# Kernel tuning notes

Measured on AMD Instinct MI355X. Metric: run time of the kernel, lower is better.

## Reference

```python
import jax, jax.numpy as jnp
import numpy as np

NUM_NEG = 100
TEMP = 0.05
EPS = 1e-12  # matches F.normalize eps


def _l2norm(x):
    n = jnp.sqrt(jnp.sum(x * x, axis=-1, keepdims=True))
    return x / jnp.maximum(n, EPS)


def setup_inputs() -> dict:
    key = jax.random.key(0)
    k1, k2, k3, k4, k5, k6 = jax.random.split(key, 6)
    B, S, D = 1024, 50, 64
    NUM_ITEMS = 100000  # table has NUM_ITEMS+1 rows (row 0 = padding)
    N = B * S
    return {
        "output_embeddings": jax.random.normal(k1, (B, S, D), dtype=jnp.float32),
        "target_ids": jax.random.randint(k2, (B, S), 1, NUM_ITEMS + 1, dtype=jnp.int64)
                      if jax.config.jax_enable_x64 else
                      jax.random.randint(k2, (B, S), 1, NUM_ITEMS + 1).astype(jnp.int32),
        "all_item_embeddings": jax.random.normal(k3, (NUM_ITEMS + 1, D), dtype=jnp.float32),
        "supervision_weights": jax.random.uniform(k4, (B, S), dtype=jnp.float32),
        "neg_indices": jax.random.randint(k5, (N, NUM_NEG), 1, NUM_ITEMS + 1).astype(jnp.int32),
        "alt_neg_indices": jax.random.randint(k6, (N, NUM_NEG), 1, NUM_ITEMS + 1).astype(jnp.int32),
    }


def reference(output_embeddings, target_ids, all_item_embeddings,
              supervision_weights, neg_indices, alt_neg_indices):
    B, S, D = output_embeddings.shape
    flat_out = output_embeddings.reshape(-1, D)            # [N, D]
    flat_tgt = target_ids.reshape(-1)                       # [N]
    flat_w = supervision_weights.reshape(-1)                # [N]
    valid = flat_w > 0

    vo = _l2norm(flat_out)                                  # [N, D]
    items = _l2norm(all_item_embeddings)                    # [V, D]

    pos_e = items[flat_tgt]                                 # [N, D]
    pos_logit = jnp.sum(vo * pos_e, axis=1)                 # [N]

    # resample negatives that collide with the positive target
    neg = jnp.where(neg_indices != flat_tgt[:, None], neg_indices, alt_neg_indices)
    neg_e = items[neg]                                      # [N, K, D]
    neg_logits = jnp.einsum('nd,nkd->nk', vo, neg_e)        # [N, K]

    logits = jnp.concatenate([pos_logit[:, None], neg_logits], axis=1) / TEMP
    # cross-entropy with label 0 == logsumexp - positive logit
    loss_per = jax.nn.logsumexp(logits, axis=1) - logits[:, 0]

    wm = jnp.where(valid, flat_w, 0.0)
    return jnp.sum(loss_per * wm) / jnp.sum(wm)
```

## Files before the change

### kernel.cpp

```cpp
#include <hip/hip_runtime.h>


#define D_DIM 64
#define K_NEG 100
#define INV_TEMP 20.0f
#define MAX_LOGIT 20.0f
#define LOG2E 1.4426950408889634f
#define LN2 0.6931471805599453f
#define MAXL2 28.853900817779268f

#define NBLK_MAIN 2048
#define NBLK_NORM 512
#define NSLOT 128

typedef float fv2 __attribute__((ext_vector_type(2)));

__device__ __forceinline__ void gload_lds16(const void* g, void* l) {
  __builtin_amdgcn_global_load_lds(
      (const __attribute__((address_space(1))) unsigned int*)g,
      (__attribute__((address_space(3))) unsigned int*)l, 16, 0, 0);
}
__device__ __forceinline__ void gload_lds4(const void* g, void* l) {
  __builtin_amdgcn_global_load_lds(
      (const __attribute__((address_space(1))) unsigned int*)g,
      (__attribute__((address_space(3))) unsigned int*)l, 4, 0, 0);
}

__global__ __launch_bounds__(256) void normalize_kernel(
    const float* __restrict__ items, unsigned int* __restrict__ tab, int V) {
  const int lane = threadIdx.x & 63;
  const int wid  = threadIdx.x >> 6;
  const int g = lane >> 4, q = lane & 15;
  const int waveId = blockIdx.x * 4 + wid;
  const int nWaves = gridDim.x * 4;
  for (int base = waveId * 4; base < V; base += nWaves * 4) {
    const int r = base + g;
    const bool act = (r < V);
    float4 x = make_float4(0.f, 0.f, 0.f, 0.f);
    if (act) x = *reinterpret_cast<const float4*>(items + (size_t)r * D_DIM + q * 4);
    float ss = x.x * x.x + x.y * x.y + x.z * x.z + x.w * x.w;
    ss += __shfl_xor(ss, 1);
    ss += __shfl_xor(ss, 2);
    ss += __shfl_xor(ss, 4);
    ss += __shfl_xor(ss, 8);
    const float inv = 1.0f / fmaxf(sqrtf(ss), 1e-12f);
    if (act) {
      int u = 0;
      u = __builtin_amdgcn_cvt_pk_fp8_f32(x.x * inv, x.y * inv, u, false);
      u = __builtin_amdgcn_cvt_pk_fp8_f32(x.z * inv, x.w * inv, u, true);
      tab[(size_t)r * 16 + q] = (unsigned int)u;
    }
  }
}

__global__ __launch_bounds__(256) void loss_kernel(
    const float* __restrict__ oe,
    const int*   __restrict__ tgt,
    const unsigned int* __restrict__ tab,
    const float* __restrict__ wgt,
    const int*   __restrict__ negi,
    const int*   __restrict__ alti,
    float2*      __restrict__ partials,
    int N) {
  __shared__ uint4 s_items[2][NSLOT * 4];
  __shared__ float s_q[2][D_DIM];
  __shared__ float s_red[2][4];
  __shared__ float s_pos[2];

  const int tid  = threadIdx.x;
  const int lane = tid & 63;
  const int wid  = tid >> 6;
  const int sub  = lane >> 2;
  const int qd   = lane & 3;
  const int G    = gridDim.x;

  const int i1 = wid;
  const int i2 = wid + 4;
  const int s1 = 16 * i1 + sub;
  const int s2 = 16 * i2 + sub;
  const bool has2 = (wid <= 2) && (s2 <= K_NEG);

  float num = 0.f, den = 0.f;
  int r = blockIdx.x;

  int ndB1 = 0, ndB2 = 0, tN = 0;
  float wC = 0.f, wN = 0.f;

  auto LOADIDX = [&](int rowS, int& d1, int& d2) {
    const int* nr = negi + (size_t)rowS * K_NEG;
    d1 = (s1 > 0) ? __builtin_nontemporal_load(nr + (s1 - 1)) : 0;
    d2 = has2 ? __builtin_nontemporal_load(nr + (s2 - 1)) : 0;
  };

  auto STAGE = [&](int rowS, int nb, int d1, int d2, int tS) {
    const int* ar = alti + (size_t)rowS * K_NEG;
    int v1 = (s1 == 0) ? tS : d1;
    if (s1 > 0 && v1 == tS) v1 = ar[s1 - 1];
    gload_lds16(tab + (size_t)v1 * 16 + qd * 4, &s_items[nb][64 * i1]);
    if (has2) {
      int v2 = d2;
      if (v2 == tS) v2 = ar[s2 - 1];
      gload_lds16(tab + (size_t)v2 * 16 + qd * 4, &s_items[nb][64 * i2]);
    }
    if (wid == 3) gload_lds4(oe + (size_t)rowS * D_DIM + lane, &s_q[nb][0]);
  };

  if (r < N) {
    int d1, d2;
    LOADIDX(r, d1, d2);
    const int t0 = tgt[r];
    wC = wgt[r];
    STAGE(r, 0, d1, d2, t0);
    const int r1 = r + G;
    if (r1 < N) {
      LOADIDX(r1, ndB1, ndB2);
      tN = tgt[r1];
      wN = wgt[r1];
    }
  }
  __syncthreads();

  int cur = 0;
  while (r < N) {
    const int r1 = r + G, r2 = r + 2 * G;
    if (r1 < N) STAGE(r1, cur ^ 1, ndB1, ndB2, tN);
    int nd1n = 0, nd2n = 0, tn2 = 0;
    float wn2 = 0.f;
    if (r2 < N) {
      LOADIDX(r2, nd1n, nd2n);
      tn2 = tgt[r2];
      wn2 = wgt[r2];
    }

    {
      const float4* qp = reinterpret_cast<const float4*>(&s_q[cur][qd * 16]);
      const float4 x0 = qp[0], x1 = qp[1], x2 = qp[2], x3 = qp[3];
      const fv2 qa0 = {x0.x, x0.y}, qa1 = {x0.z, x0.w};
      const fv2 qa2 = {x1.x, x1.y}, qa3 = {x1.z, x1.w};
      const fv2 qa4 = {x2.x, x2.y}, qa5 = {x2.z, x2.w};
      const fv2 qa6 = {x3.x, x3.y}, qa7 = {x3.z, x3.w};

      fv2 ss2 = qa0 * qa0;
      ss2 += qa1 * qa1;
      ss2 += qa2 * qa2;
      ss2 += qa3 * qa3;
      ss2 += qa4 * qa4;
      ss2 += qa5 * qa5;
      ss2 += qa6 * qa6;
      ss2 += qa7 * qa7;
      float ss = ss2[0] + ss2[1];
      ss += __shfl_xor(ss, 1);
      ss += __shfl_xor(ss, 2);
      const float inv_o = 1.0f / fmaxf(sqrtf(ss), 1e-12f);
      const float scale = inv_o * INV_TEMP;
      const float sc2 = scale * LOG2E;

      float sacc = 0.f;
#pragma unroll
      for (int p = 0; p < 2; ++p) {
        const int s = p * 64 + wid * 16 + sub;
        const uint4 rv = s_items[cur][s * 4 + qd];
        fv2 acc;
        acc  = qa0 * __builtin_amdgcn_cvt_pk_f32_fp8((int)rv.x, false);
        acc += qa1 * __builtin_amdgcn_cvt_pk_f32_fp8((int)rv.x, true);
        acc += qa2 * __builtin_amdgcn_cvt_pk_f32_fp8((int)rv.y, false);
        acc += qa3 * __builtin_amdgcn_cvt_pk_f32_fp8((int)rv.y, true);
        acc += qa4 * __builtin_amdgcn_cvt_pk_f32_fp8((int)rv.z, false);
        acc += qa5 * __builtin_amdgcn_cvt_pk_f32_fp8((int)rv.z, true);
        acc += qa6 * __builtin_amdgcn_cvt_pk_f32_fp8((int)rv.w, false);
        acc += qa7 * __builtin_amdgcn_cvt_pk_f32_fp8((int)rv.w, true);
        float d = acc[0] + acc[1];
        d += __shfl_xor(d, 1);
        d += __shfl_xor(d, 2);
        if (p == 0 && tid == 0) s_pos[cur] = d * scale;
        const float e = exp2f(fmaf(d, sc2, -MAXL2));
        sacc += (s <= K_NEG && qd == 0) ? e : 0.f;
      }
      sacc += __shfl_xor(sacc, 4);
      sacc += __shfl_xor(sacc, 8);
      sacc += __shfl_xor(sacc, 16);
      sacc += __shfl_xor(sacc, 32);
      if (lane == 0) s_red[cur][wid] = sacc;
    }

    __syncthreads();

    if (tid == 0) {
      const float S = s_red[cur][0] + s_red[cur][1] + s_red[cur][2] + s_red[cur][3];
      const float lse = log2f(S) * LN2 + MAX_LOGIT;
      const float loss = lse - s_pos[cur];
      if (wC > 0.f) {
        num += loss * wC;
        den += wC;
      }
    }

    wC = wN; wN = wn2;
    ndB1 = nd1n; ndB2 = nd2n; tN = tn2;
    cur ^= 1;
    r += G;
  }

  if (tid == 0) partials[blockIdx.x] = make_float2(num, den);
}

__global__ __launch_bounds__(256) void finish_kernel(
    const float2* __restrict__ partials, int nblk, float* __restrict__ out) {
  float num = 0.f, den = 0.f;
  for (int i = threadIdx.x; i < nblk; i += 256) {
    const float2 p = partials[i];
    num += p.x;
    den += p.y;
  }
#pragma unroll
  for (int m = 1; m < 64; m <<= 1) {
    num += __shfl_xor(num, m);
    den += __shfl_xor(den, m);
  }
  __shared__ float2 red[4];
  const int wid = threadIdx.x >> 6;
  const int lane = threadIdx.x & 63;
  if (lane == 0) red[wid] = make_float2(num, den);
  __syncthreads();
  if (threadIdx.x == 0) {
    float n = 0.f, d = 0.f;
#pragma unroll
    for (int i = 0; i < 4; ++i) { n += red[i].x; d += red[i].y; }
    out[0] = n / d;
  }
}

extern "C" void kernel_launch(void* const* d_in, const int* in_sizes, int n_in,
                              void* d_out, int out_size, void* d_ws, size_t ws_size,
                              hipStream_t stream) {
  const float* oe    = (const float*)d_in[0];
  const int*   tgt   = (const int*)  d_in[1];
  const float* items = (const float*)d_in[2];
  const float* wgt   = (const float*)d_in[3];
  const int*   negi  = (const int*)  d_in[4];
  const int*   alti  = (const int*)  d_in[5];

  const int N = in_sizes[0] / D_DIM;
  const int V = in_sizes[2] / D_DIM;

  unsigned int* tab = (unsigned int*)d_ws;
  size_t off = ((size_t)V * 16 * sizeof(unsigned int) + 255) & ~(size_t)255;
  float2* partials = (float2*)((char*)d_ws + off);

  normalize_kernel<<<NBLK_NORM, 256, 0, stream>>>(items, tab, V);
  loss_kernel<<<NBLK_MAIN, 256, 0, stream>>>(oe, tgt, tab, wgt, negi, alti,
                                             partials, N);
  finish_kernel<<<1, 256, 0, stream>>>(partials, NBLK_MAIN, (float*)d_out);
}
```

Before: 79.06 us.

## Split fp8 item table into two half-dimension tables processed in two passes

The normalized fp8 table is stored as two 32-dim half tables, and the loss kernel makes two passes over each block's rows, one per half. Partial dot products and query sums of squares are kept in shared memory between passes. Each pass's gather working set is half the size, so it should fit better in L2/MALL during random gathers. The cost is reading the index arrays twice, more syncs, and a grid sized to at most 25 rows per block instead of a fixed 2048 blocks.

```diff
diff --git a/kernel.cpp b/kernel.cpp
--- a/kernel.cpp
+++ b/kernel.cpp
@@ -9,9 +9,10 @@
 #define LN2 0.6931471805599453f
 #define MAXL2 28.853900817779268f
 
-#define NBLK_MAIN 2048
-#define NBLK_NORM 512
+#define NBLK_NORM 1024
+#define MAXR 25
 #define NSLOT 128
+#define PSTRIDE 104
 
 typedef float fv2 __attribute__((ext_vector_type(2)));
 
@@ -20,14 +21,10 @@
       (const __attribute__((address_space(1))) unsigned int*)g,
       (__attribute__((address_space(3))) unsigned int*)l, 16, 0, 0);
 }
-__device__ __forceinline__ void gload_lds4(const void* g, void* l) {
-  __builtin_amdgcn_global_load_lds(
-      (const __attribute__((address_space(1))) unsigned int*)g,
-      (__attribute__((address_space(3))) unsigned int*)l, 4, 0, 0);
-}
 
 __global__ __launch_bounds__(256) void normalize_kernel(
-    const float* __restrict__ items, unsigned int* __restrict__ tab, int V) {
+    const float* __restrict__ items, unsigned int* __restrict__ tabA,
+    unsigned int* __restrict__ tabB, int V) {
   const int lane = threadIdx.x & 63;
   const int wid  = threadIdx.x >> 6;
   const int g = lane >> 4, q = lane & 15;
@@ -48,92 +45,79 @@
       int u = 0;
       u = __builtin_amdgcn_cvt_pk_fp8_f32(x.x * inv, x.y * inv, u, false);
       u = __builtin_amdgcn_cvt_pk_fp8_f32(x.z * inv, x.w * inv, u, true);
-      tab[(size_t)r * 16 + q] = (unsigned int)u;
+      unsigned int* t = (q < 8) ? (tabA + (size_t)r * 8 + q)
+                                : (tabB + (size_t)r * 8 + (q - 8));
+      *t = (unsigned int)u;
     }
   }
 }
 
-__global__ __launch_bounds__(256) void loss_kernel(
+__global__ __launch_bounds__(256, 8) void loss_kernel(
     const float* __restrict__ oe,
     const int*   __restrict__ tgt,
-    const unsigned int* __restrict__ tab,
+    const unsigned int* __restrict__ tabA,
+    const unsigned int* __restrict__ tabB,
     const float* __restrict__ wgt,
     const int*   __restrict__ negi,
     const int*   __restrict__ alti,
     float2*      __restrict__ partials,
     int N) {
-  __shared__ uint4 s_items[2][NSLOT * 4];
-  __shared__ float s_q[2][D_DIM];
+  __shared__ uint4 s_items[2][NSLOT * 2];
+  __shared__ float s_q[2][32];
+  __shared__ float s_part[MAXR][PSTRIDE];
+  __shared__ float s_ss[MAXR];
   __shared__ float s_red[2][4];
-  __shared__ float s_pos[2];
 
   const int tid  = threadIdx.x;
   const int lane = tid & 63;
   const int wid  = tid >> 6;
-  const int sub  = lane >> 2;
-  const int qd   = lane & 3;
-  const int G    = gridDim.x;
-
-  const int i1 = wid;
-  const int i2 = wid + 4;
-  const int s1 = 16 * i1 + sub;
-  const int s2 = 16 * i2 + sub;
-  const bool has2 = (wid <= 2) && (s2 <= K_NEG);
+  const int s    = tid >> 1;
+  const int h    = tid & 1;
+  const int j    = s - 1;
+  const bool sval = (s <= K_NEG);
+  const bool nval = sval && (s >= 1);
+  const int G  = gridDim.x;
+  const int r0 = blockIdx.x;
+  const int nr = (N - r0 + G - 1) / G;
 
   float num = 0.f, den = 0.f;
-  int r = blockIdx.x;
-
-  int ndB1 = 0, ndB2 = 0, tN = 0;
-  float wC = 0.f, wN = 0.f;
-
-  auto LOADIDX = [&](int rowS, int& d1, int& d2) {
-    const int* nr = negi + (size_t)rowS * K_NEG;
-    d1 = (s1 > 0) ? __builtin_nontemporal_load(nr + (s1 - 1)) : 0;
-    d2 = has2 ? __builtin_nontemporal_load(nr + (s2 - 1)) : 0;
-  };
-
-  auto STAGE = [&](int rowS, int nb, int d1, int d2, int tS) {
-    const int* ar = alti + (size_t)rowS * K_NEG;
-    int v1 = (s1 == 0) ? tS : d1;
-    if (s1 > 0 && v1 == tS) v1 = ar[s1 - 1];
-    gload_lds16(tab + (size_t)v1 * 16 + qd * 4, &s_items[nb][64 * i1]);
-    if (has2) {
-      int v2 = d2;
-      if (v2 == tS) v2 = ar[s2 - 1];
-      gload_lds16(tab + (size_t)v2 * 16 + qd * 4, &s_items[nb][64 * i2]);
+
+  uint4* const dst0 = &s_items[0][wid * 64];
+  uint4* const dst1 = &s_items[1][wid * 64];
+
+  auto run_phase = [&](const unsigned int* __restrict__ TAB, int P, bool FIN) {
+    auto STAGE = [&](int rowS, int nb, int rawneg, int tS) {
+      int v = (s == 0) ? tS : rawneg;
+      if (nval && v == tS) v = alti[(size_t)rowS * K_NEG + j];
+      if (sval) gload_lds16(TAB + (size_t)v * 8 + h * 4, nb ? dst1 : dst0);
+      if (wid == 3 && lane < 8)
+        gload_lds16(oe + (size_t)rowS * D_DIM + P * 32 + lane * 4,
+                    nb ? &s_q[1][0] : &s_q[0][0]);
+    };
+
+    int rawneg = 0, tS = 0;
+    if (nval) rawneg = __builtin_nontemporal_load(negi + (size_t)r0 * K_NEG + j);
+    tS = tgt[r0];
+    STAGE(r0, 0, rawneg, tS);
+    if (nr > 1) {
+      const int r1 = r0 + G;
+      rawneg = nval ? __builtin_nontemporal_load(negi + (size_t)r1 * K_NEG + j) : 0;
+      tS = tgt[r1];
     }
-    if (wid == 3) gload_lds4(oe + (size_t)rowS * D_DIM + lane, &s_q[nb][0]);
-  };
-
-  if (r < N) {
-    int d1, d2;
-    LOADIDX(r, d1, d2);
-    const int t0 = tgt[r];
-    wC = wgt[r];
-    STAGE(r, 0, d1, d2, t0);
-    const int r1 = r + G;
-    if (r1 < N) {
-      LOADIDX(r1, ndB1, ndB2);
-      tN = tgt[r1];
-      wN = wgt[r1];
-    }
-  }
-  __syncthreads();
-
-  int cur = 0;
-  while (r < N) {
-    const int r1 = r + G, r2 = r + 2 * G;
-    if (r1 < N) STAGE(r1, cur ^ 1, ndB1, ndB2, tN);
-    int nd1n = 0, nd2n = 0, tn2 = 0;
-    float wn2 = 0.f;
-    if (r2 < N) {
-      LOADIDX(r2, nd1n, nd2n);
-      tn2 = tgt[r2];
-      wn2 = wgt[r2];
-    }
-
-    {
-      const float4* qp = reinterpret_cast<const float4*>(&s_q[cur][qd * 16]);
+    __syncthreads();
+
+    int buf = 0;
+    for (int k = 0; k < nr; ++k) {
+      const int r = r0 + k * G;
+      if (k + 1 < nr) STAGE(r0 + (k + 1) * G, buf ^ 1, rawneg, tS);
+      if (k + 2 < nr) {
+        const int r2 = r0 + (k + 2) * G;
+        rawneg = nval ? __builtin_nontemporal_load(negi + (size_t)r2 * K_NEG + j) : 0;
+        tS = tgt[r2];
+      }
+      const float w = FIN ? wgt[r] : 0.f;
+
+      const float4* qp = reinterpret_cast<const float4*>(&s_q[buf][h * 16]);
       const float4 x0 = qp[0], x1 = qp[1], x2 = qp[2], x3 = qp[3];
       const fv2 qa0 = {x0.x, x0.y}, qa1 = {x0.z, x0.w};
       const fv2 qa2 = {x1.x, x1.y}, qa3 = {x1.z, x1.w};
@@ -148,58 +132,60 @@
       ss2 += qa5 * qa5;
       ss2 += qa6 * qa6;
       ss2 += qa7 * qa7;
-      float ss = ss2[0] + ss2[1];
-      ss += __shfl_xor(ss, 1);
-      ss += __shfl_xor(ss, 2);
-      const float inv_o = 1.0f / fmaxf(sqrtf(ss), 1e-12f);
-      const float scale = inv_o * INV_TEMP;
-      const float sc2 = scale * LOG2E;
-
-      float sacc = 0.f;
-#pragma unroll
-      for (int p = 0; p < 2; ++p) {
-        const int s = p * 64 + wid * 16 + sub;
-        const uint4 rv = s_items[cur][s * 4 + qd];
-        fv2 acc;
-        acc  = qa0 * __builtin_amdgcn_cvt_pk_f32_fp8((int)rv.x, false);
-        acc += qa1 * __builtin_amdgcn_cvt_pk_f32_fp8((int)rv.x, true);
-        acc += qa2 * __builtin_amdgcn_cvt_pk_f32_fp8((int)rv.y, false);
-        acc += qa3 * __builtin_amdgcn_cvt_pk_f32_fp8((int)rv.y, true);
-        acc += qa4 * __builtin_amdgcn_cvt_pk_f32_fp8((int)rv.z, false);
-        acc += qa5 * __builtin_amdgcn_cvt_pk_f32_fp8((int)rv.z, true);
-        acc += qa6 * __builtin_amdgcn_cvt_pk_f32_fp8((int)rv.w, false);
-        acc += qa7 * __builtin_amdgcn_cvt_pk_f32_fp8((int)rv.w, true);
-        float d = acc[0] + acc[1];
-        d += __shfl_xor(d, 1);
-        d += __shfl_xor(d, 2);
-        if (p == 0 && tid == 0) s_pos[cur] = d * scale;
-        const float e = exp2f(fmaf(d, sc2, -MAXL2));
-        sacc += (s <= K_NEG && qd == 0) ? e : 0.f;
+      float ssh = ss2[0] + ss2[1];
+      ssh += __shfl_xor(ssh, 1);
+
+      const uint4 rv = s_items[buf][tid];
+      fv2 acc;
+      acc  = qa0 * __builtin_amdgcn_cvt_pk_f32_fp8((int)rv.x, false);
+      acc += qa1 * __builtin_amdgcn_cvt_pk_f32_fp8((int)rv.x, true);
+      acc += qa2 * __builtin_amdgcn_cvt_pk_f32_fp8((int)rv.y, false);
+      acc += qa3 * __builtin_amdgcn_cvt_pk_f32_fp8((int)rv.y, true);
+      acc += qa4 * __builtin_amdgcn_cvt_pk_f32_fp8((int)rv.z, false);
+      acc += qa5 * __builtin_amdgcn_cvt_pk_f32_fp8((int)rv.z, true);
+      acc += qa6 * __builtin_amdgcn_cvt_pk_f32_fp8((int)rv.w, false);
+      acc += qa7 * __builtin_amdgcn_cvt_pk_f32_fp8((int)rv.w, true);
+      float d = acc[0] + acc[1];
+      d += __shfl_xor(d, 1);
+
+      float pos = 0.f;
+      if (!FIN) {
+        if (h == 0 && sval) s_part[k][s] = d;
+        if (tid == 0) s_ss[k] = ssh;
+      } else {
+        const float sstot = ssh + s_ss[k];
+        const float sc = INV_TEMP / fmaxf(sqrtf(sstot), 1e-12f);
+        float tot = 0.f;
+        if (sval) tot = s_part[k][s] + d;
+        float e = 0.f;
+        if (h == 0 && sval) e = exp2f(fmaf(tot, sc * LOG2E, -MAXL2));
+        e += __shfl_xor(e, 1);
+        e += __shfl_xor(e, 2);
+        e += __shfl_xor(e, 4);
+        e += __shfl_xor(e, 8);
+        e += __shfl_xor(e, 16);
+        e += __shfl_xor(e, 32);
+        if (lane == 0) s_red[buf][wid] = e;
+        if (tid == 0) pos = tot * sc;
       }
-      sacc += __shfl_xor(sacc, 4);
-      sacc += __shfl_xor(sacc, 8);
-      sacc += __shfl_xor(sacc, 16);
-      sacc += __shfl_xor(sacc, 32);
-      if (lane == 0) s_red[cur][wid] = sacc;
+
+      __syncthreads();
+
+      if (FIN && tid == 0) {
+        const float S = s_red[buf][0] + s_red[buf][1] + s_red[buf][2] + s_red[buf][3];
+        const float lse = log2f(S) * LN2 + MAX_LOGIT;
+        const float loss = lse - pos;
+        if (w > 0.f) {
+          num += loss * w;
+          den += w;
+        }
+      }
+      buf ^= 1;
     }
-
-    __syncthreads();
-
-    if (tid == 0) {
-      const float S = s_red[cur][0] + s_red[cur][1] + s_red[cur][2] + s_red[cur][3];
-      const float lse = log2f(S) * LN2 + MAX_LOGIT;
-      const float loss = lse - s_pos[cur];
-      if (wC > 0.f) {
-        num += loss * wC;
-        den += wC;
-      }
-    }
-
-    wC = wN; wN = wn2;
-    ndB1 = nd1n; ndB2 = nd2n; tN = tn2;
-    cur ^= 1;
-    r += G;
-  }
+  };
+
+  run_phase(tabA, 0, false);
+  run_phase(tabB, 1, true);
 
   if (tid == 0) partials[blockIdx.x] = make_float2(num, den);
 }
@@ -242,13 +228,15 @@
 
   const int N = in_sizes[0] / D_DIM;
   const int V = in_sizes[2] / D_DIM;
-
-  unsigned int* tab = (unsigned int*)d_ws;
+  const int G = (N + MAXR - 1) / MAXR;
+
+  unsigned int* tabA = (unsigned int*)d_ws;
+  unsigned int* tabB = tabA + (size_t)V * 8;
   size_t off = ((size_t)V * 16 * sizeof(unsigned int) + 255) & ~(size_t)255;
   float2* partials = (float2*)((char*)d_ws + off);
 
-  normalize_kernel<<<NBLK_NORM, 256, 0, stream>>>(items, tab, V);
-  loss_kernel<<<NBLK_MAIN, 256, 0, stream>>>(oe, tgt, tab, wgt, negi, alti,
-                                             partials, N);
-  finish_kernel<<<1, 256, 0, stream>>>(partials, NBLK_MAIN, (float*)d_out);
-}
+  normalize_kernel<<<NBLK_NORM, 256, 0, stream>>>(items, tabA, tabB, V);
+  loss_kernel<<<G, 256, 0, stream>>>(oe, tgt, tabA, tabB, wgt, negi, alti,
+                                     partials, N);
+  finish_kernel<<<1, 256, 0, stream>>>(partials, G, (float*)d_out);
+}
```

Result: slower. 111.0 us (+40.4%).
